# Kernel optimization log

Hardware: AMD Instinct MI355X
Metric: run time of the kernel (lower is better)

## Reference

```python
import jax, jax.numpy as jnp
import numpy as np

VAT = 57      # vat_tokens
ACT = 56      # action_num (KV slice start for cross-attn)
H = 16        # num_heads
NG = 3        # n_groups for num_non_act == 768


def setup_inputs() -> dict:
    key = jax.random.key(0)
    ks = jax.random.split(key, 6)
    B, N, C = 64, 825, 1024
    s = 0.02
    return {
        "x": jax.random.normal(ks[0], (B, N, C), dtype=jnp.float32),
        "W_qkv_non": jax.random.normal(ks[1], (C, 3 * C), dtype=jnp.float32) * s,
        "W_q_act": jax.random.normal(ks[2], (C, C), dtype=jnp.float32) * s,
        "W_kv_act": jax.random.normal(ks[3], (C, 2 * C), dtype=jnp.float32) * s,
        "W_proj_non": jax.random.normal(ks[4], (C, C), dtype=jnp.float32) * s,
        "b_proj_non": jnp.zeros((C,), dtype=jnp.float32),
        "W_proj_act": jax.random.normal(ks[5], (C, C), dtype=jnp.float32) * s,
        "b_proj_act": jnp.zeros((C,), dtype=jnp.float32),
    }


def reference(x, W_qkv_non, W_q_act, W_kv_act, W_proj_non, b_proj_non,
              W_proj_act, b_proj_act):
    B, N, C = x.shape
    d = C // H
    scale = d ** -0.5
    nna = N - VAT              # num non-act tokens (768)
    gs = nna // NG             # group size (256)

    # --- grouped windowed self-attention over non-act tokens ---
    non = x[:, VAT:].reshape(B, NG, gs, C)
    qkv = (non @ W_qkv_non).reshape(B, NG, gs, 3, H, d)
    q, k, v = jnp.moveaxis(qkv, 3, 0)           # each [B, NG, gs, H, d]
    q = q.transpose(0, 1, 3, 2, 4)              # [B, NG, H, gs, d]
    k = k.transpose(0, 1, 3, 2, 4)
    v = v.transpose(0, 1, 3, 2, 4)
    attn = jax.nn.softmax(jnp.einsum('bghqd,bghkd->bghqk', q, k) * scale, axis=-1)
    x_non = jnp.einsum('bghqk,bghkd->bghqd', attn, v)
    x_non = x_non.transpose(0, 1, 3, 2, 4).reshape(B, nna, C)

    # --- cross-attention: act queries attend to KV subset [ACT:] of all tokens ---
    q_act = (x[:, :VAT] @ W_q_act).reshape(B, VAT, H, d).transpose(0, 2, 1, 3)
    kv = (x @ W_kv_act).reshape(B, N, 2, H, d)
    k_act = kv[:, ACT:, 0].transpose(0, 2, 1, 3)   # [B, H, N-ACT, d]
    v_act = kv[:, ACT:, 1].transpose(0, 2, 1, 3)
    attn_a = jax.nn.softmax(jnp.einsum('bhqd,bhkd->bhqk', q_act, k_act) * scale, axis=-1)
    x_act = jnp.einsum('bhqk,bhkd->bhqd', attn_a, v_act)
    x_act = x_act.transpose(0, 2, 1, 3).reshape(B, VAT, C)

    # --- output projections + concat [act, non] ---
    x_non = x_non @ W_proj_non + b_proj_non
    x_act = x_act @ W_proj_act + b_proj_act
    return jnp.concatenate([x_act, x_non], axis=1)
```

## Files before the change

kernel.cpp:

```cpp
#include <hip/hip_runtime.h>
#include <stdint.h>


typedef __attribute__((ext_vector_type(8))) unsigned short u16x8;
typedef __attribute__((ext_vector_type(8))) _Float16 f16x8;
typedef __attribute__((ext_vector_type(4))) float f32x4;

__device__ __forceinline__ unsigned short f2h(float f) {
  _Float16 h = (_Float16)f;
  return __builtin_bit_cast(unsigned short, h);
}

__device__ __forceinline__ void mfma16(f32x4& d, u16x8 a, u16x8 b) {
  asm("v_mfma_f32_16x16x32_f16 %0, %1, %2, %0" : "+v"(d) : "v"(a), "v"(b));
}

__device__ __forceinline__ void async16(void* lds_p, const void* g) {
  __builtin_amdgcn_global_load_lds(
      (const __attribute__((address_space(1))) unsigned int*)g,
      (__attribute__((address_space(3))) unsigned int*)lds_p, 16, 0, 0);
}

__device__ __forceinline__ int swz(int row, int bcol) {
  return (row << 7) + (bcol ^ ((row & 7) << 4));
}

static constexpr size_t OFF_XB   = 0;
static constexpr size_t OFF_QKV  = 108134400;
static constexpr size_t OFF_KV   = 410124288;
static constexpr size_t OFF_QACT = 611713024;
static constexpr size_t OFF_ANON = 619184128;
static constexpr size_t OFF_AACT = 719847424;
static constexpr size_t OFF_WQKV = 727318528;
static constexpr size_t OFF_WKV  = 733609984;
static constexpr size_t OFF_WQ   = 737804288;
static constexpr size_t OFF_WPN  = 739901440;
static constexpr size_t OFF_WPA  = 741998592;

__global__ __launch_bounds__(256) void k_cast(const float* __restrict__ in,
                                              unsigned short* __restrict__ outp,
                                              int n4) {
  int i = blockIdx.x * 256 + threadIdx.x;
  if (i >= n4) return;
  float4 v = ((const float4*)in)[i];
  uint2 w;
  w.x = (unsigned)f2h(v.x) | ((unsigned)f2h(v.y) << 16);
  w.y = (unsigned)f2h(v.z) | ((unsigned)f2h(v.w) << 16);
  ((uint2*)outp)[i] = w;
}

__global__ __launch_bounds__(256) void k_tc(const float* __restrict__ W,
                                            unsigned short* __restrict__ Wt,
                                            int Nc) {
  __shared__ float ts[32][33];
  int n0 = blockIdx.x * 32, k0 = blockIdx.y * 32;
  int tx = threadIdx.x & 31, ty = threadIdx.x >> 5;
#pragma unroll
  for (int i = 0; i < 4; i++) {
    int k = ty + i * 8;
    ts[k][tx] = W[(size_t)(k0 + k) * Nc + n0 + tx];
  }
  __syncthreads();
#pragma unroll
  for (int i = 0; i < 4; i++) {
    int n = ty + i * 8;
    Wt[(size_t)(n0 + n) * 1024 + k0 + tx] = f2h(ts[tx][n]);
  }
}

template <int EPI>
__global__ __launch_bounds__(512, 2) void k_gemm256(
    const unsigned short* __restrict__ A, const unsigned short* __restrict__ Bt,
    const float* __restrict__ bias, void* __restrict__ outp,
    int M, int NTN, int arpb, int aoff, int ldo, int orpb, int ooff) {
  extern __shared__ char lds[];
  int tid = threadIdx.x, lane = tid & 63, wid = tid >> 6;
  int fr = lane & 15, fg = lane >> 4;

  int nwg = gridDim.x;
  int q8 = nwg >> 3, r8 = nwg & 7;
  int xcd = blockIdx.x & 7, idx = blockIdx.x >> 3;
  int wg = (xcd < r8 ? xcd * (q8 + 1) : r8 * (q8 + 1) + (xcd - r8) * q8) + idx;
  int mt = wg / NTN, nt = wg - mt * NTN;
  int r0 = mt << 8, n0 = nt << 8;

  const unsigned short* pA[2][2];
  const unsigned short* pB[2][2];
#pragma unroll
  for (int j = 0; j < 2; j++) {
    int rc = (wid * 2 + j) * 8 + (lane >> 3);
    int cc = (lane & 7) ^ (rc & 7);
#pragma unroll
    for (int a = 0; a < 2; a++) {
      int row = (rc >> 6) * 128 + a * 64 + (rc & 63);
      int r = r0 + row;
      if (r >= M) r = M - 1;
      size_t gr;
      if (arpb > 0) { int bb = r / arpb; gr = (size_t)bb * 825 + aoff + (r - bb * arpb); }
      else gr = (size_t)r;
      pA[a][j] = A + gr * 1024 + cc * 8;
    }
#pragma unroll
    for (int b = 0; b < 2; b++) {
      int n = ((rc >> 5) & 3) * 64 + b * 32 + (rc & 31);
      pB[b][j] = Bt + (size_t)(n0 + n) * 1024 + cc * 8;
    }
  }

  int wr = wid >> 2, wc = wid & 3;
  int ch0 = fg ^ (fr & 7);
  int aoff0 = (wr * 64 + fr) * 128 + ch0 * 16;
  int boff0 = (wc * 32 + fr) * 128 + ch0 * 16;

  u16x8 afr[8], bf0[4], bf1[4];
  f32x4 acc[8][4] = {};

#define BAR  asm volatile("s_barrier" ::: "memory")
#define LGKM0 { asm volatile("s_waitcnt lgkmcnt(0)" ::: "memory"); \
                __builtin_amdgcn_sched_barrier(0); }
#define VM6  asm volatile("s_waitcnt vmcnt(6)" ::: "memory")
#define VM0  asm volatile("s_waitcnt vmcnt(0)" ::: "memory")

  auto LDA = [&](int d, int a) {
    char* base = lds + d * 65536 + a * 16384;
#pragma unroll
    for (int mm = 0; mm < 4; mm++)
#pragma unroll
      for (int ks = 0; ks < 2; ks++)
        afr[mm * 2 + ks] = *(const u16x8*)(base + mm * 2048 + (aoff0 ^ (ks * 64)));
  };
  auto LDB = [&](int d, int b, u16x8* bf) {
    char* base = lds + d * 65536 + 32768 + b * 16384;
#pragma unroll
    for (int nn = 0; nn < 2; nn++)
#pragma unroll
      for (int ks = 0; ks < 2; ks++)
        bf[nn * 2 + ks] = *(const u16x8*)(base + nn * 2048 + (boff0 ^ (ks * 64)));
  };
  auto STAGE_A = [&](int d, int a, int t) {
#pragma unroll
    for (int j = 0; j < 2; j++)
      async16(lds + d * 65536 + a * 16384 + ((wid * 2 + j) << 10), pA[a][j] + t * 64);
  };
  auto STAGE_B = [&](int d, int b, int t) {
#pragma unroll
    for (int j = 0; j < 2; j++)
      async16(lds + d * 65536 + 32768 + b * 16384 + ((wid * 2 + j) << 10), pB[b][j] + t * 64);
  };
  auto CLUSTER = [&](int a, int b, u16x8* bf) {
    __builtin_amdgcn_s_setprio(1);
#pragma unroll
    for (int mm = 0; mm < 4; mm++)
#pragma unroll
      for (int nn = 0; nn < 2; nn++)
#pragma unroll
        for (int ks = 0; ks < 2; ks++)
          mfma16(acc[a * 4 + mm][b * 2 + nn], afr[mm * 2 + ks], bf[nn * 2 + ks]);
    __builtin_amdgcn_sched_barrier(0);
    __builtin_amdgcn_s_setprio(0);
  };

  STAGE_A(0, 0, 0); STAGE_B(0, 0, 0); STAGE_B(0, 1, 0); STAGE_A(0, 1, 0);
  STAGE_A(1, 0, 1); STAGE_B(1, 0, 1); STAGE_B(1, 1, 1);
  VM6; BAR;

#pragma unroll 1
  for (int i = 0; i < 8; i++) {
    bool nl = (i < 7);
    int t1 = 2 * i + 1, t2 = 2 * i + 2, t3 = 2 * i + 3;
    LDA(0, 0); LDB(0, 0, bf0);
    STAGE_A(1, 1, t1);
    asm volatile("s_waitcnt lgkmcnt(8)" ::: "memory");
    BAR; LGKM0; CLUSTER(0, 0, bf0); BAR;
    LDB(0, 1, bf1);
    if (nl) STAGE_A(0, 0, t2);
    BAR; LGKM0; CLUSTER(0, 1, bf1); BAR;
    LDA(0, 1);
    if (nl) STAGE_B(0, 0, t2);
    BAR; LGKM0; CLUSTER(1, 0, bf0); BAR;
    if (nl) STAGE_B(0, 1, t2);
    BAR; CLUSTER(1, 1, bf1);
    if (nl) { VM6; } else { VM0; }
    BAR;
    LDA(1, 0); LDB(1, 0, bf0);
    if (nl) STAGE_A(0, 1, t2);
    asm volatile("s_waitcnt lgkmcnt(8)" ::: "memory");
    BAR; LGKM0; CLUSTER(0, 0, bf0); BAR;
    LDB(1, 1, bf1);
    if (nl) STAGE_A(1, 0, t3);
    BAR; LGKM0; CLUSTER(0, 1, bf1); BAR;
    LDA(1, 1);
    if (nl) STAGE_B(1, 0, t3);
    BAR; LGKM0; CLUSTER(1, 0, bf0); BAR;
    if (nl) STAGE_B(1, 1, t3);
    BAR; CLUSTER(1, 1, bf1);
    if (nl) { VM6; } else { VM0; }
    BAR;
  }
#undef BAR
#undef LGKM0
#undef VM6
#undef VM0

  int coln[4];
#pragma unroll
  for (int n = 0; n < 4; n++)
    coln[n] = n0 + wc * 64 + (n >> 1) * 32 + (n & 1) * 16 + fr;
  if (EPI == 0) {
    unsigned short* o = (unsigned short*)outp;
#pragma unroll
    for (int m = 0; m < 8; m++)
#pragma unroll
      for (int reg = 0; reg < 4; reg++) {
        int r = r0 + wr * 128 + (m >> 2) * 64 + (m & 3) * 16 + (lane >> 4) * 4 + reg;
        if (r < M) {
          size_t base = (size_t)r * ldo;
#pragma unroll
          for (int n = 0; n < 4; n++) o[base + coln[n]] = f2h(acc[m][n][reg]);
        }
      }
  } else {
    float* o = (float*)outp;
#pragma unroll
    for (int m = 0; m < 8; m++)
#pragma unroll
      for (int reg = 0; reg < 4; reg++) {
        int r = r0 + wr * 128 + (m >> 2) * 64 + (m & 3) * 16 + (lane >> 4) * 4 + reg;
        if (r < M) {
          int bb = r / orpb;
          size_t orow = (size_t)bb * 825 + ooff + (r - bb * orpb);
          size_t base = orow * 1024;
#pragma unroll
          for (int n = 0; n < 4; n++)
            o[base + coln[n]] = acc[m][n][reg] + bias[coln[n]];
        }
      }
  }
}

template <int EPI>
__global__ __launch_bounds__(256, 2) void k_gemm(
    const unsigned short* __restrict__ A, const unsigned short* __restrict__ Bt,
    const float* __restrict__ bias, void* __restrict__ outp,
    int M, int Nn, int arpb, int aoff, int ldo, int orpb, int ooff) {
  __shared__ __align__(16) unsigned short As[128 * 32];
  __shared__ __align__(16) unsigned short Bs[128 * 32];
  int tid = threadIdx.x, lane = tid & 63, wid = tid >> 6;
  int NT = Nn >> 7;
  int mt = blockIdx.x / NT, nt = blockIdx.x - mt * NT;
  int r0 = mt << 7, n0 = nt << 7;

  const unsigned short* aptr[2];
  const unsigned short* bptr[2];
#pragma unroll
  for (int i = 0; i < 2; i++) {
    int c = tid + (i << 8);
    int r = r0 + (c >> 2);
    if (r >= M) r = M - 1;
    size_t gr;
    if (arpb > 0) { int bb = r / arpb; gr = (size_t)bb * 825 + aoff + (r - bb * arpb); }
    else gr = (size_t)r;
    aptr[i] = A + gr * 1024 + (c & 3) * 8;
    bptr[i] = Bt + (size_t)(n0 + (c >> 2)) * 1024 + (c & 3) * 8;
  }
  char* AsB = (char*)As;
  char* BsB = (char*)Bs;
  int wr = wid >> 1, wc = wid & 1;
  int fr = lane & 15, fcol = (lane >> 4) * 16;
  f32x4 acc[4][4] = {};

  for (int kk = 0; kk < 1024; kk += 32) {
    async16(AsB + (wid << 10), aptr[0] + kk);
    async16(AsB + 4096 + (wid << 10), aptr[1] + kk);
    async16(BsB + (wid << 10), bptr[0] + kk);
    async16(BsB + 4096 + (wid << 10), bptr[1] + kk);
    __syncthreads();
    u16x8 af[4], bfv[4];
#pragma unroll
    for (int m = 0; m < 4; m++)
      af[m] = *(const u16x8*)(AsB + (wr * 64 + m * 16 + fr) * 64 + fcol);
#pragma unroll
    for (int n = 0; n < 4; n++)
      bfv[n] = *(const u16x8*)(BsB + (wc * 64 + n * 16 + fr) * 64 + fcol);
#pragma unroll
    for (int m = 0; m < 4; m++)
#pragma unroll
      for (int n = 0; n < 4; n++) mfma16(acc[m][n], af[m], bfv[n]);
    __syncthreads();
  }

  int cb = wc * 64 + fr;
  int rb = wr * 64 + (lane >> 4) * 4;
  if (EPI == 0) {
    unsigned short* o = (unsigned short*)outp;
#pragma unroll
    for (int m = 0; m < 4; m++)
#pragma unroll
      for (int reg = 0; reg < 4; reg++) {
        int r = r0 + rb + m * 16 + reg;
        if (r < M) {
          size_t base = (size_t)r * ldo + n0 + cb;
#pragma unroll
          for (int n = 0; n < 4; n++) o[base + n * 16] = f2h(acc[m][n][reg]);
        }
      }
  } else {
    float* o = (float*)outp;
#pragma unroll
    for (int m = 0; m < 4; m++)
#pragma unroll
      for (int reg = 0; reg < 4; reg++) {
        int r = r0 + rb + m * 16 + reg;
        if (r < M) {
          int bb = r / orpb;
          size_t orow = (size_t)bb * 825 + ooff + (r - bb * orpb);
          size_t base = orow * 1024 + n0 + cb;
#pragma unroll
          for (int n = 0; n < 4; n++)
            o[base + n * 16] = acc[m][n][reg] + bias[n0 + cb + n * 16];
        }
      }
  }
}

__global__ __launch_bounds__(256, 2) void k_attn_non(
    const unsigned short* __restrict__ qkv, unsigned short* __restrict__ aout) {
  int bid = blockIdx.x;
  int h = bid & 15, t = bid >> 4;
  int g = t % 3, b = t / 3;
  int tid = threadIdx.x, lane = tid & 63, wid = tid >> 6;
  int fr = lane & 15, fg = lane >> 4;
  size_t rowbase = (size_t)(b * 768 + g * 256);
  const unsigned short* Qb = qkv + rowbase * 3072 + h * 64;
  const unsigned short* Kb = Qb + 1024;
  const unsigned short* Vb = Qb + 2048;

  __shared__ __align__(16) unsigned short Ks[64 * 64];
  __shared__ __align__(16) unsigned short Vts[64 * 64];
  __shared__ __align__(16) unsigned short Ps[4][64 * 64];
  char* KsB = (char*)Ks;
  char* VtB = (char*)Vts;
  char* Pw = (char*)Ps[wid];

  int qr = wid * 64;
  u16x8 qf[4][2];
#pragma unroll
  for (int mq = 0; mq < 4; mq++)
#pragma unroll
    for (int ks = 0; ks < 2; ks++)
      qf[mq][ks] = *(const u16x8*)(Qb + (size_t)(qr + mq * 16 + fr) * 3072 + ks * 32 + fg * 8);

  f32x4 o[4][4] = {};
  float mrun[4], lrun[4];
#pragma unroll
  for (int mq = 0; mq < 4; mq++) { mrun[mq] = -1e30f; lrun[mq] = 0.f; }
  const float c1 = 0.125f * 1.44269504089f;

  for (int c = 0; c < 4; c++) {
    __syncthreads();
#pragma unroll
    for (int i = 0; i < 2; i++) {
      int cc = tid + i * 256;
      int row = cc >> 3, c16 = cc & 7;
      u16x8 kvv = *(const u16x8*)(Kb + (size_t)(c * 64 + row) * 3072 + c16 * 8);
      *(u16x8*)(KsB + swz(row, c16 * 16)) = kvv;
      u16x8 vv = *(const u16x8*)(Vb + (size_t)(c * 64 + row) * 3072 + c16 * 8);
#pragma unroll
      for (int j = 0; j < 8; j++)
        *(unsigned short*)(VtB + swz(c16 * 8 + j, row * 2)) = vv[j];
    }
    __syncthreads();

    f32x4 s[4][4] = {};
#pragma unroll
    for (int ks = 0; ks < 2; ks++) {
      u16x8 kf[4];
#pragma unroll
      for (int kt = 0; kt < 4; kt++)
        kf[kt] = *(const u16x8*)(KsB + swz(kt * 16 + fr, ks * 64 + fg * 16));
#pragma unroll
      for (int kt = 0; kt < 4; kt++)
#pragma unroll
        for (int mq = 0; mq < 4; mq++) mfma16(s[kt][mq], kf[kt], qf[mq][ks]);
    }
#pragma unroll
    for (int kt = 0; kt < 4; kt++)
#pragma unroll
      for (int mq = 0; mq < 4; mq++) s[kt][mq] *= c1;

#pragma unroll
    for (int mq = 0; mq < 4; mq++) {
      float v = -1e30f;
#pragma unroll
      for (int kt = 0; kt < 4; kt++)
#pragma unroll
        for (int reg = 0; reg < 4; reg++) v = fmaxf(v, s[kt][mq][reg]);
      v = fmaxf(v, __shfl_xor(v, 16));
      v = fmaxf(v, __shfl_xor(v, 32));
      float mn = fmaxf(mrun[mq], v);
      float alpha = exp2f(mrun[mq] - mn);
      mrun[mq] = mn;
      int q = mq * 16 + fr;
      float rs = 0.f;
#pragma unroll
      for (int kt = 0; kt < 4; kt++) {
        f32x4 p;
#pragma unroll
        for (int reg = 0; reg < 4; reg++) p[reg] = exp2f(s[kt][mq][reg] - mn);
        rs += p[0] + p[1] + p[2] + p[3];
        uint2 w;
        w.x = (unsigned)f2h(p[0]) | ((unsigned)f2h(p[1]) << 16);
        w.y = (unsigned)f2h(p[2]) | ((unsigned)f2h(p[3]) << 16);
        *(uint2*)(Pw + swz(q, kt * 32 + fg * 8)) = w;
      }
      rs += __shfl_xor(rs, 16);
      rs += __shfl_xor(rs, 32);
      lrun[mq] = lrun[mq] * alpha + rs;
#pragma unroll
      for (int dt = 0; dt < 4; dt++) o[dt][mq] *= alpha;
    }
    asm volatile("s_waitcnt lgkmcnt(0)" ::: "memory");
#pragma unroll
    for (int ks = 0; ks < 2; ks++) {
      u16x8 vf[4], pf[4];
#pragma unroll
      for (int dt = 0; dt < 4; dt++)
        vf[dt] = *(const u16x8*)(VtB + swz(dt * 16 + fr, ks * 64 + fg * 16));
#pragma unroll
      for (int mq = 0; mq < 4; mq++)
        pf[mq] = *(const u16x8*)(Pw + swz(mq * 16 + fr, ks * 64 + fg * 16));
#pragma unroll
      for (int dt = 0; dt < 4; dt++)
#pragma unroll
        for (int mq = 0; mq < 4; mq++) mfma16(o[dt][mq], vf[dt], pf[mq]);
    }
  }

#pragma unroll
  for (int mq = 0; mq < 4; mq++) {
    float rl = 1.0f / lrun[mq];
    size_t row = rowbase + qr + mq * 16 + fr;
#pragma unroll
    for (int dt = 0; dt < 4; dt++) {
      uint2 w;
      w.x = (unsigned)f2h(o[dt][mq][0] * rl) | ((unsigned)f2h(o[dt][mq][1] * rl) << 16);
      w.y = (unsigned)f2h(o[dt][mq][2] * rl) | ((unsigned)f2h(o[dt][mq][3] * rl) << 16);
      *(uint2*)(aout + row * 1024 + h * 64 + dt * 16 + fg * 4) = w;
    }
  }
}

__global__ __launch_bounds__(256, 2) void k_attn_act(
    const unsigned short* __restrict__ qa, const unsigned short* __restrict__ kv,
    unsigned short* __restrict__ aout) {
  int bid = blockIdx.x;
  int h = bid & 15, b = bid >> 4;
  int tid = threadIdx.x, lane = tid & 63, wid = tid >> 6;
  int fr = lane & 15, fg = lane >> 4;
  const unsigned short* Qb = qa + (size_t)b * 57 * 1024 + h * 64;
  const unsigned short* Kb = kv + (size_t)b * 769 * 2048 + h * 64;
  const unsigned short* Vb = Kb + 1024;

  __shared__ __align__(16) unsigned short Ks[4][64 * 64];
  __shared__ __align__(16) unsigned short Vts[4][64 * 64];
  __shared__ __align__(16) unsigned short Ps[4][64 * 64];
  __shared__ float Ml[4][64], Ll[4][64];
  char* Kw = (char*)Ks[wid];
  char* Vw = (char*)Vts[wid];
  char* Pw = (char*)Ps[wid];

  u16x8 qf[4][2];
#pragma unroll
  for (int mq = 0; mq < 4; mq++) {
    int q = mq * 16 + fr;
    if (q > 56) q = 56;
#pragma unroll
    for (int ks = 0; ks < 2; ks++)
      qf[mq][ks] = *(const u16x8*)(Qb + (size_t)q * 1024 + ks * 32 + fg * 8);
  }
  f32x4 o[4][4] = {};
  float mrun[4], lrun[4];
#pragma unroll
  for (int mq = 0; mq < 4; mq++) { mrun[mq] = -1e30f; lrun[mq] = 0.f; }
  const float c1 = 0.125f * 1.44269504089f;

  for (int c = wid; c < 13; c += 4) {
    int kc0 = c * 64;
#pragma unroll
    for (int i = 0; i < 8; i++) {
      int cc = lane + i * 64;
      int row = cc >> 3, c16 = cc & 7;
      int krow = kc0 + row;
      if (krow > 768) krow = 768;
      u16x8 kvv = *(const u16x8*)(Kb + (size_t)krow * 2048 + c16 * 8);
      *(u16x8*)(Kw + swz(row, c16 * 16)) = kvv;
      u16x8 vv = *(const u16x8*)(Vb + (size_t)krow * 2048 + c16 * 8);
#pragma unroll
      for (int j = 0; j < 8; j++)
        *(unsigned short*)(Vw + swz(c16 * 8 + j, row * 2)) = vv[j];
    }
    asm volatile("s_waitcnt lgkmcnt(0)" ::: "memory");

    f32x4 s[4][4] = {};
#pragma unroll
    for (int ks = 0; ks < 2; ks++) {
      u16x8 kf[4];
#pragma unroll
      for (int kt = 0; kt < 4; kt++)
        kf[kt] = *(const u16x8*)(Kw + swz(kt * 16 + fr, ks * 64 + fg * 16));
#pragma unroll
      for (int kt = 0; kt < 4; kt++)
#pragma unroll
        for (int mq = 0; mq < 4; mq++) mfma16(s[kt][mq], kf[kt], qf[mq][ks]);
    }
#pragma unroll
    for (int kt = 0; kt < 4; kt++)
#pragma unroll
      for (int mq = 0; mq < 4; mq++) s[kt][mq] *= c1;
    if (kc0 + 64 > 769) {
#pragma unroll
      for (int kt = 0; kt < 4; kt++)
#pragma unroll
        for (int reg = 0; reg < 4; reg++)
          if (kc0 + kt * 16 + fg * 4 + reg >= 769)
#pragma unroll
            for (int mq = 0; mq < 4; mq++) s[kt][mq][reg] = -1e30f;
    }

#pragma unroll
    for (int mq = 0; mq < 4; mq++) {
      float v = -1e30f;
#pragma unroll
      for (int kt = 0; kt < 4; kt++)
#pragma unroll
        for (int reg = 0; reg < 4; reg++) v = fmaxf(v, s[kt][mq][reg]);
      v = fmaxf(v, __shfl_xor(v, 16));
      v = fmaxf(v, __shfl_xor(v, 32));
      float mn = fmaxf(mrun[mq], v);
      float alpha = exp2f(mrun[mq] - mn);
      mrun[mq] = mn;
      int q = mq * 16 + fr;
      float rs = 0.f;
#pragma unroll
      for (int kt = 0; kt < 4; kt++) {
        f32x4 p;
#pragma unroll
        for (int reg = 0; reg < 4; reg++) p[reg] = exp2f(s[kt][mq][reg] - mn);
        rs += p[0] + p[1] + p[2] + p[3];
        uint2 w;
        w.x = (unsigned)f2h(p[0]) | ((unsigned)f2h(p[1]) << 16);
        w.y = (unsigned)f2h(p[2]) | ((unsigned)f2h(p[3]) << 16);
        *(uint2*)(Pw + swz(q, kt * 32 + fg * 8)) = w;
      }
      rs += __shfl_xor(rs, 16);
      rs += __shfl_xor(rs, 32);
      lrun[mq] = lrun[mq] * alpha + rs;
#pragma unroll
      for (int dt = 0; dt < 4; dt++) o[dt][mq] *= alpha;
    }
    asm volatile("s_waitcnt lgkmcnt(0)" ::: "memory");
#pragma unroll
    for (int ks = 0; ks < 2; ks++) {
      u16x8 vf[4], pf[4];
#pragma unroll
      for (int dt = 0; dt < 4; dt++)
        vf[dt] = *(const u16x8*)(Vw + swz(dt * 16 + fr, ks * 64 + fg * 16));
#pragma unroll
      for (int mq = 0; mq < 4; mq++)
        pf[mq] = *(const u16x8*)(Pw + swz(mq * 16 + fr, ks * 64 + fg * 16));
#pragma unroll
      for (int dt = 0; dt < 4; dt++)
#pragma unroll
        for (int mq = 0; mq < 4; mq++) mfma16(o[dt][mq], vf[dt], pf[mq]);
    }
  }

  __syncthreads();
  if (fg == 0) {
#pragma unroll
    for (int mq = 0; mq < 4; mq++) {
      Ml[wid][mq * 16 + fr] = mrun[mq];
      Ll[wid][mq * 16 + fr] = lrun[mq];
    }
  }
  __syncthreads();
  float* Oac = (float*)&Ks[0][0];
  for (int i = tid; i < 4096; i += 256) Oac[i] = 0.f;
  __syncthreads();
  for (int w = 0; w < 4; w++) {
    if (wid == w) {
#pragma unroll
      for (int mq = 0; mq < 4; mq++) {
        int q = mq * 16 + fr;
        float Mq = fmaxf(fmaxf(Ml[0][q], Ml[1][q]), fmaxf(Ml[2][q], Ml[3][q]));
        float f = exp2f(mrun[mq] - Mq);
#pragma unroll
        for (int dt = 0; dt < 4; dt++) {
          int d = dt * 16 + fg * 4;
#pragma unroll
          for (int reg = 0; reg < 4; reg++)
            Oac[(d + reg) * 64 + q] += o[dt][mq][reg] * f;
        }
      }
    }
    __syncthreads();
  }
  for (int i = tid; i < 4096; i += 256) {
    int d = i >> 6, q = i & 63;
    if (q < 57) {
      float Mq = fmaxf(fmaxf(Ml[0][q], Ml[1][q]), fmaxf(Ml[2][q], Ml[3][q]));
      float Lq = Ll[0][q] * exp2f(Ml[0][q] - Mq) + Ll[1][q] * exp2f(Ml[1][q] - Mq) +
                 Ll[2][q] * exp2f(Ml[2][q] - Mq) + Ll[3][q] * exp2f(Ml[3][q] - Mq);
      aout[(size_t)(b * 57 + q) * 1024 + h * 64 + d] = f2h(Oac[i] / Lq);
    }
  }
}

extern "C" void kernel_launch(void* const* d_in, const int* in_sizes, int n_in,
                              void* d_out, int out_size, void* d_ws, size_t ws_size,
                              hipStream_t stream) {
  const float* x    = (const float*)d_in[0];
  const float* Wqkv = (const float*)d_in[1];
  const float* Wq   = (const float*)d_in[2];
  const float* Wkv  = (const float*)d_in[3];
  const float* Wpn  = (const float*)d_in[4];
  const float* bpn  = (const float*)d_in[5];
  const float* Wpa  = (const float*)d_in[6];
  const float* bpa  = (const float*)d_in[7];
  float* out = (float*)d_out;
  char* ws = (char*)d_ws;

  unsigned short* xb   = (unsigned short*)(ws + OFF_XB);
  unsigned short* qkv  = (unsigned short*)(ws + OFF_QKV);
  unsigned short* kvb  = (unsigned short*)(ws + OFF_KV);
  unsigned short* qact = (unsigned short*)(ws + OFF_QACT);
  unsigned short* anon = (unsigned short*)(ws + OFF_ANON);
  unsigned short* aact = (unsigned short*)(ws + OFF_AACT);
  unsigned short* WtQKV = (unsigned short*)(ws + OFF_WQKV);
  unsigned short* WtKV  = (unsigned short*)(ws + OFF_WKV);
  unsigned short* WtQ   = (unsigned short*)(ws + OFF_WQ);
  unsigned short* WtPN  = (unsigned short*)(ws + OFF_WPN);
  unsigned short* WtPA  = (unsigned short*)(ws + OFF_WPA);

  hipFuncSetAttribute((const void*)k_gemm256<0>,
                      hipFuncAttributeMaxDynamicSharedMemorySize, 131072);
  hipFuncSetAttribute((const void*)k_gemm256<1>,
                      hipFuncAttributeMaxDynamicSharedMemorySize, 131072);

  k_cast<<<52800, 256, 0, stream>>>(x, xb, 13516800);
  k_tc<<<dim3(96, 32), 256, 0, stream>>>(Wqkv, WtQKV, 3072);
  k_tc<<<dim3(64, 32), 256, 0, stream>>>(Wkv, WtKV, 2048);
  k_tc<<<dim3(32, 32), 256, 0, stream>>>(Wq, WtQ, 1024);
  k_tc<<<dim3(32, 32), 256, 0, stream>>>(Wpn, WtPN, 1024);
  k_tc<<<dim3(32, 32), 256, 0, stream>>>(Wpa, WtPA, 1024);

  k_gemm256<0><<<192 * 12, 512, 131072, stream>>>(xb, WtQKV, nullptr, qkv,
                                                  49152, 12, 768, 57, 3072, 0, 0);
  k_gemm256<0><<<193 * 8, 512, 131072, stream>>>(xb, WtKV, nullptr, kvb,
                                                 49216, 8, 769, 56, 2048, 0, 0);
  k_gemm<0><<<29 * 8, 256, 0, stream>>>(xb, WtQ, nullptr, qact,
                                        3648, 1024, 57, 0, 1024, 0, 0);

  k_attn_non<<<64 * 3 * 16, 256, 0, stream>>>(qkv, anon);
  k_attn_act<<<64 * 16, 256, 0, stream>>>(qact, kvb, aact);

  k_gemm256<1><<<192 * 4, 512, 131072, stream>>>(anon, WtPN, bpn, out,
                                                 49152, 4, 0, 0, 1024, 768, 57);
  k_gemm<1><<<29 * 8, 256, 0, stream>>>(aact, WtPA, bpa, out,
                                        3648, 1024, 0, 0, 1024, 57, 0);
}
```

Measured before the change: 1.092 ms.

## Trim GEMM loop barriers and pack V transpose stores into 32-bit writes

The GEMM main loop drops several workgroup barriers and the partial lgkmcnt waits between MFMA clusters, which cuts synchronization stalls. Both attention kernels change the V-tile transpose into LDS so that each thread loads two adjacent key rows and writes packed 32-bit pairs instead of single 16-bit values. That halves the number of LDS store instructions. Removing barriers risks LDS races if a staged async load overwrites a buffer another wave is still reading.

Measured after the change: 1.063 ms. 1.03x faster.

```diff
diff --git a/kernel.cpp b/kernel.cpp
--- a/kernel.cpp
+++ b/kernel.cpp
@@ -3,7 +3,6 @@
 
 
 typedef __attribute__((ext_vector_type(8))) unsigned short u16x8;
-typedef __attribute__((ext_vector_type(8))) _Float16 f16x8;
 typedef __attribute__((ext_vector_type(4))) float f32x4;
 
 __device__ __forceinline__ unsigned short f2h(float f) {
@@ -170,30 +169,28 @@
     int t1 = 2 * i + 1, t2 = 2 * i + 2, t3 = 2 * i + 3;
     LDA(0, 0); LDB(0, 0, bf0);
     STAGE_A(1, 1, t1);
-    asm volatile("s_waitcnt lgkmcnt(8)" ::: "memory");
-    BAR; LGKM0; CLUSTER(0, 0, bf0); BAR;
+    LGKM0; CLUSTER(0, 0, bf0); BAR;
     LDB(0, 1, bf1);
     if (nl) STAGE_A(0, 0, t2);
-    BAR; LGKM0; CLUSTER(0, 1, bf1); BAR;
+    LGKM0; CLUSTER(0, 1, bf1);
     LDA(0, 1);
     if (nl) STAGE_B(0, 0, t2);
-    BAR; LGKM0; CLUSTER(1, 0, bf0); BAR;
+    LGKM0; CLUSTER(1, 0, bf0); BAR;
     if (nl) STAGE_B(0, 1, t2);
-    BAR; CLUSTER(1, 1, bf1);
+    CLUSTER(1, 1, bf1);
     if (nl) { VM6; } else { VM0; }
     BAR;
     LDA(1, 0); LDB(1, 0, bf0);
     if (nl) STAGE_A(0, 1, t2);
-    asm volatile("s_waitcnt lgkmcnt(8)" ::: "memory");
-    BAR; LGKM0; CLUSTER(0, 0, bf0); BAR;
+    LGKM0; CLUSTER(0, 0, bf0); BAR;
     LDB(1, 1, bf1);
     if (nl) STAGE_A(1, 0, t3);
-    BAR; LGKM0; CLUSTER(0, 1, bf1); BAR;
+    LGKM0; CLUSTER(0, 1, bf1);
     LDA(1, 1);
     if (nl) STAGE_B(1, 0, t3);
-    BAR; LGKM0; CLUSTER(1, 0, bf0); BAR;
+    LGKM0; CLUSTER(1, 0, bf0); BAR;
     if (nl) STAGE_B(1, 1, t3);
-    BAR; CLUSTER(1, 1, bf1);
+    CLUSTER(1, 1, bf1);
     if (nl) { VM6; } else { VM0; }
     BAR;
   }
@@ -356,6 +353,7 @@
   for (int mq = 0; mq < 4; mq++) { mrun[mq] = -1e30f; lrun[mq] = 0.f; }
   const float c1 = 0.125f * 1.44269504089f;
 
+  int vpr = tid >> 3, vcc = tid & 7;
   for (int c = 0; c < 4; c++) {
     __syncthreads();
 #pragma unroll
@@ -364,10 +362,15 @@
       int row = cc >> 3, c16 = cc & 7;
       u16x8 kvv = *(const u16x8*)(Kb + (size_t)(c * 64 + row) * 3072 + c16 * 8);
       *(u16x8*)(KsB + swz(row, c16 * 16)) = kvv;
-      u16x8 vv = *(const u16x8*)(Vb + (size_t)(c * 64 + row) * 3072 + c16 * 8);
-#pragma unroll
-      for (int j = 0; j < 8; j++)
-        *(unsigned short*)(VtB + swz(c16 * 8 + j, row * 2)) = vv[j];
+    }
+    {
+      u16x8 v0 = *(const u16x8*)(Vb + (size_t)(c * 64 + 2 * vpr) * 3072 + vcc * 8);
+      u16x8 v1 = *(const u16x8*)(Vb + (size_t)(c * 64 + 2 * vpr + 1) * 3072 + vcc * 8);
+#pragma unroll
+      for (int j = 0; j < 8; j++) {
+        unsigned pk = (unsigned)v0[j] | ((unsigned)v1[j] << 16);
+        *(unsigned*)(VtB + swz(vcc * 8 + j, 4 * vpr)) = pk;
+      }
     }
     __syncthreads();
 
@@ -494,10 +497,21 @@
       if (krow > 768) krow = 768;
       u16x8 kvv = *(const u16x8*)(Kb + (size_t)krow * 2048 + c16 * 8);
       *(u16x8*)(Kw + swz(row, c16 * 16)) = kvv;
-      u16x8 vv = *(const u16x8*)(Vb + (size_t)krow * 2048 + c16 * 8);
-#pragma unroll
-      for (int j = 0; j < 8; j++)
-        *(unsigned short*)(Vw + swz(c16 * 8 + j, row * 2)) = vv[j];
+    }
+#pragma unroll
+    for (int i = 0; i < 4; i++) {
+      int idx = lane + i * 64;
+      int pr = idx >> 3, cv = idx & 7;
+      int kr0 = kc0 + 2 * pr, kr1 = kc0 + 2 * pr + 1;
+      if (kr0 > 768) kr0 = 768;
+      if (kr1 > 768) kr1 = 768;
+      u16x8 v0 = *(const u16x8*)(Vb + (size_t)kr0 * 2048 + cv * 8);
+      u16x8 v1 = *(const u16x8*)(Vb + (size_t)kr1 * 2048 + cv * 8);
+#pragma unroll
+      for (int j = 0; j < 8; j++) {
+        unsigned pk = (unsigned)v0[j] | ((unsigned)v1[j] << 16);
+        *(unsigned*)(Vw + swz(cv * 8 + j, 4 * pr)) = pk;
+      }
     }
     asm volatile("s_waitcnt lgkmcnt(0)" ::: "memory");
 
```
